# Performance work log

Hardware: AMD Instinct MI355X
Metric: run time of the kernel (lower is better)

Reference implementation:

```python
import jax, jax.numpy as jnp
import numpy as np

OUT_DIM = 130

def _gru_cell(x, h, wih, whh, bih, bhh):
    # torch.nn.GRUCell math
    gi = x @ wih.T + bih            # [N, 3H]
    gh = h @ whh.T + bhh            # [N, 3H]
    ir, iz, inn = jnp.split(gi, 3, axis=-1)
    hr, hz, hn = jnp.split(gh, 3, axis=-1)
    r = jax.nn.sigmoid(ir + hr)
    z = jax.nn.sigmoid(iz + hz)
    n = jnp.tanh(inn + r * hn)
    return (1.0 - z) * n + z * h


def setup_inputs() -> dict:
    key = jax.random.key(0)
    ks = jax.random.split(key, 16)
    E, B, C, H, D = 16, 128, 512, 1024, OUT_DIM
    S = 16  # length // 2
    T = E * S
    s = 0.02
    inp = {
        "c": jax.random.normal(ks[0], (E, B, C), jnp.float32),
        "target": jax.random.normal(ks[1], (B, T, D), jnp.float32),
        "length": 32,
        "batch_size": B,
        "fc_init_w": s * jax.random.normal(ks[2], (2 * H, C), jnp.float32),
        "fc_init_b": s * jax.random.normal(ks[3], (2 * H,), jnp.float32),
        "g1_wih": s * jax.random.normal(ks[4], (3 * H, C + D), jnp.float32),
        "g1_whh": s * jax.random.normal(ks[5], (3 * H, H), jnp.float32),
        "g1_bih": s * jax.random.normal(ks[6], (3 * H,), jnp.float32),
        "g1_bhh": s * jax.random.normal(ks[7], (3 * H,), jnp.float32),
        "g2_wih": s * jax.random.normal(ks[8], (3 * H, H), jnp.float32),
        "g2_whh": s * jax.random.normal(ks[9], (3 * H, H), jnp.float32),
        "g2_bih": s * jax.random.normal(ks[10], (3 * H,), jnp.float32),
        "g2_bhh": s * jax.random.normal(ks[11], (3 * H,), jnp.float32),
        "fco_w": s * jax.random.normal(ks[12], (D, H), jnp.float32),
        "fco_b": s * jax.random.normal(ks[13], (D,), jnp.float32),
    }
    return inp


def reference(c, target, length, batch_size, fc_init_w, fc_init_b,
              g1_wih, g1_whh, g1_bih, g1_bhh,
              g2_wih, g2_whh, g2_bih, g2_bhh, fco_w, fco_b):
    E, B, C = c.shape
    H = fc_init_w.shape[0] // 2
    D = fco_w.shape[0]
    S = length // 2
    T = E * S
    # h1/h2 init per conductor embed: tanh(fc_init(embed))
    t0 = jnp.tanh(c @ fc_init_w.T + fc_init_b)           # [E,B,2H]
    h1 = t0[..., :H].reshape(E * B, H)
    h2 = t0[..., H:].reshape(E * B, H)
    # teacher-forced previous: prev[t]=0 at t=0 else target[:,t-1]
    prev = jnp.concatenate([jnp.zeros((B, 1, D), target.dtype), target[:, :T - 1]], axis=1)  # [B,T,D]
    # global step t = e*S + s -> [S, E*B, D]
    prev = prev.transpose(1, 0, 2).reshape(E, S, B, D).transpose(1, 0, 2, 3).reshape(S, E * B, D)
    cflat = c.reshape(E * B, C)

    def step(carry, prev_t):
        h1, h2 = carry
        x = jnp.concatenate([cflat, prev_t], axis=-1)    # [E*B, C+D]
        h1 = _gru_cell(x, h1, g1_wih, g1_whh, g1_bih, g1_bhh)
        h2 = _gru_cell(h1, h2, g2_wih, g2_whh, g2_bih, g2_bhh)
        y = h2 @ fco_w.T + fco_b                         # [E*B, D]
        return (h1, h2), y

    _, ys = jax.lax.scan(step, (h1, h2), prev)           # [S, E*B, D]
    ys = ys.reshape(S, E, B, D).transpose(2, 1, 0, 3).reshape(B, T, D)
    return ys
```

## Files before the change

kernel.cpp:

```cpp
#include <hip/hip_runtime.h>

typedef unsigned short u16;
typedef __attribute__((ext_vector_type(8))) short frag8;
typedef __attribute__((ext_vector_type(4))) float f32x4;
typedef __attribute__((ext_vector_type(8))) unsigned short u16x8;

typedef __attribute__((address_space(1))) const void GV;
typedef __attribute__((address_space(3))) void LV;

__device__ __forceinline__ void gl16(const u16* g, u16* l) {
  __builtin_amdgcn_global_load_lds((GV*)g, (LV*)l, 16, 0, 0);
}

__device__ __forceinline__ float b2f(u16 u) {
  union { unsigned int i; float f; } v; v.i = ((unsigned int)u) << 16; return v.f;
}
__device__ __forceinline__ u16 f2b(float f) {
  union { float f; unsigned int i; } v; v.f = f;
  unsigned int x = v.i;
  x += 0x7fffu + ((x >> 16) & 1u);
  return (u16)(x >> 16);
}
__device__ __forceinline__ float ftanh(float x) {
  float e = __expf(2.f * x);
  return 1.f - 2.f / (e + 1.f);
}

__device__ __forceinline__ void xcd_remap(int axis, int& bx, int& by) {
  const int nx = gridDim.x, ny = gridDim.y;
  const int nwg = nx * ny;
  const int bid = blockIdx.x + nx * blockIdx.y;
  const int q = nwg >> 3, r = nwg & 7;
  const int xcd = bid & 7, i = bid >> 3;
  const int rem = (xcd < r ? xcd * (q + 1) : r * (q + 1) + (xcd - r) * q) + i;
  if (axis == 0) { bx = rem / ny; by = rem - bx * ny; }
  else           { by = rem / nx; bx = rem - by * nx; }
}

__global__ void cvt3(const float* __restrict__ s0, const float* __restrict__ s1,
                     const float* __restrict__ s2, u16* __restrict__ d0,
                     u16* __restrict__ d1, u16* __restrict__ d2) {
  int i = blockIdx.x * 256 + threadIdx.x;
  int which = i / 3145728;
  int j = i - which * 3145728;
  const float* s = (which == 0) ? s0 : (which == 1 ? s1 : s2);
  u16* d = (which == 0) ? d0 : (which == 1 ? d1 : d2);
  d[j] = f2b(s[j]);
}

__global__ void cvt2(const float* __restrict__ s0, const float* __restrict__ s1,
                     u16* __restrict__ d0, u16* __restrict__ d1) {
  int i = blockIdx.x * 256 + threadIdx.x;
  if (i < 1048576) d0[i] = f2b(s0[i]);
  else             d1[i - 1048576] = f2b(s1[i - 1048576]);
}

__global__ void prep_w1(const float* __restrict__ wih, u16* __restrict__ Wc, u16* __restrict__ Wd) {
  int i = blockIdx.x * 256 + threadIdx.x;
  const int NC = 3072 * 512;
  const int ND = 3072 * 192;
  if (i < NC) {
    int n = i >> 9, k = i & 511;
    Wc[i] = f2b(wih[n * 642 + k]);
  } else if (i < NC + ND) {
    int j = i - NC;
    int n = j / 192, k = j - n * 192;
    Wd[j] = (k < 130) ? f2b(wih[n * 642 + 512 + k]) : (u16)0;
  }
}

__global__ void prep_wby(const float* __restrict__ fcow, u16* __restrict__ wby) {
  int i = blockIdx.x * 256 + threadIdx.x;
  int n = i >> 10;
  wby[i] = (n < 130) ? f2b(fcow[i]) : (u16)0;
}

__global__ void prep_prev(const float* __restrict__ target, u16* __restrict__ P) {
  int i = blockIdx.x * 256 + threadIdx.x;
  int row = i / 24;
  int c8  = i - row * 24;
  int k0 = c8 * 8;
  int t = row >> 11, m2 = row & 2047;
  int e = m2 >> 7, b = m2 & 127;
  int tt = e * 16 + t;
  u16x8 r;
  if (tt > 0 && k0 + 8 <= 130) {
    const float* trow = target + (size_t)(b * 256 + tt - 1) * 130 + k0;
#pragma unroll
    for (int q = 0; q < 8; ++q) r[q] = f2b(trow[q]);
  } else if (tt > 0 && k0 < 130) {
    const float* trow = target + (size_t)(b * 256 + tt - 1) * 130;
#pragma unroll
    for (int q = 0; q < 8; ++q) { int k = k0 + q; r[q] = (k < 130) ? f2b(trow[k]) : (u16)0; }
  } else {
#pragma unroll
    for (int q = 0; q < 8; ++q) r[q] = (u16)0;
  }
  *(u16x8*)&P[(size_t)row * 192 + k0] = r;
}

__device__ __forceinline__ void kloop3(
    const u16* gA, const u16* gB, int nk,
    u16* AsBase, u16* BsBase, int wave,
    int rdA, int rdB, f32x4 (&acc)[2][4])
{
  u16* Adst = AsBase + wave * 512;
  u16* Bdst = BsBase + wave * 512;
  gl16(gA,      Adst);        gl16(gB,      Bdst);
  gl16(gA + 32, Adst + 4096); gl16(gB + 32, Bdst + 4096);
  const u16* pA = gA + 64;
  const u16* pB = gB + 64;
  int cbuf = 0, nbuf = 2;
  for (int ks = 0; ks < nk; ++ks) {
    if (ks < nk - 1) asm volatile("s_waitcnt vmcnt(2)" : : : "memory");
    else             asm volatile("s_waitcnt vmcnt(0)" : : : "memory");
    __builtin_amdgcn_s_barrier();
    __builtin_amdgcn_sched_barrier(0);
    if (ks + 2 < nk) {
      gl16(pA, Adst + nbuf * 4096);
      gl16(pB, Bdst + nbuf * 4096);
      pA += 32; pB += 32;
    }
    const u16* Ab = AsBase + cbuf * 4096;
    const u16* Bb = BsBase + cbuf * 4096;
    frag8 af[2], bfr[4];
#pragma unroll
    for (int i = 0; i < 2; ++i)
      af[i] = *(const frag8*)&Ab[rdA + i * 512];
#pragma unroll
    for (int j = 0; j < 4; ++j)
      bfr[j] = *(const frag8*)&Bb[rdB + j * 512];
#pragma unroll
    for (int i = 0; i < 2; ++i)
#pragma unroll
      for (int j = 0; j < 4; ++j)
        acc[i][j] = __builtin_amdgcn_mfma_f32_16x16x32_bf16(af[i], bfr[j], acc[i][j], 0, 0, 0);
    cbuf = (cbuf == 2) ? 0 : cbuf + 1;
    nbuf = (nbuf == 2) ? 0 : nbuf + 1;
  }
}

__global__ __launch_bounds__(512, 6) void gemm_bt(
    const u16* __restrict__ A, int lda,
    const u16* __restrict__ B0, const u16* __restrict__ B1, int ldb, int n_split,
    int N, int K, int mode, int tstep, int axis,
    const float* __restrict__ bias0, const float* __restrict__ bias1,
    u16* __restrict__ out0, u16* __restrict__ out1,
    const u16* __restrict__ addmat,
    float* __restrict__ fout0, float* __restrict__ fout1)
{
  __shared__ u16 As[3 * 4096];
  __shared__ u16 Bs[3 * 4096];

  int bx, by;
  xcd_remap(axis, bx, by);

  const int tid = threadIdx.x;
  const int wave = tid >> 6;
  const int lane = tid & 63;
  const int m0 = by * 128;
  const int n0 = bx * 128;
  const int wm = (wave & 3) * 32;
  const int wn = (wave >> 2) * 64;
  const int lr = lane & 15;
  const int lq = lane >> 4;
  const int sw = (lr >> 1) & 3;
  const int rdA = (wm + lr) * 32 + ((lq ^ sw) << 3);
  const int rdB = (wn + lr) * 32 + ((lq ^ sw) << 3);

  const u16* Bsel;
  int nb0;
  if (n0 < n_split) { Bsel = B0; nb0 = n0; }
  else              { Bsel = B1; nb0 = n0 - n_split; }

  f32x4 acc[2][4] = {};

  const int srow_g = wave * 16 + (lane >> 2);
  const int scol_g = (((lane & 3) ^ ((lane >> 3) & 3)) << 3);
  const u16* gA = &A[(size_t)(m0 + srow_g) * lda + scol_g];
  const u16* gB = &Bsel[(size_t)(nb0 + srow_g) * ldb + scol_g];

  kloop3(gA, gB, K >> 5, As, Bs, wave, rdA, rdB, acc);

#pragma unroll
  for (int i = 0; i < 2; ++i) {
#pragma unroll
    for (int r = 0; r < 4; ++r) {
      int m = m0 + wm + i * 16 + lq * 4 + r;
#pragma unroll
      for (int j = 0; j < 4; ++j) {
        int n = n0 + wn + j * 16 + lr;
        float v = acc[i][j][r];
        if (mode == 1) {
          float t = ftanh(v + bias0[n]);
          if (n < 1024) { fout0[(size_t)m * 1024 + n] = t;          out0[(size_t)m * 1024 + n] = f2b(t); }
          else          { fout1[(size_t)m * 1024 + (n - 1024)] = t; out1[(size_t)m * 1024 + (n - 1024)] = f2b(t); }
        } else if (mode == 2) {
          out0[(size_t)m * 3072 + n] = f2b(v + b2f(addmat[(size_t)(m & 2047) * 3072 + n]));
        } else if (mode == 3) {
          if (n < 3072) out0[(size_t)m * 3072 + n] = f2b(v + bias0[n]);
          else          out1[(size_t)m * 3072 + (n - 3072)] = f2b(v + bias1[n - 3072]);
        } else {
          if (n < 3072) {
            out0[(size_t)m * 3072 + n] = f2b(v + bias0[n]);
          } else if (n < 3202) {
            int d = n - 3072;
            int b = m & 127, e = m >> 7;
            fout0[(size_t)((b << 8) + (e << 4) + tstep) * 130 + d] = v + bias1[d];
          }
        }
      }
    }
  }
}

__global__ __launch_bounds__(512, 6) void gemm_init(
    const u16* __restrict__ cbf, const u16* __restrict__ h1b, const u16* __restrict__ h2b,
    const u16* __restrict__ Wc, const u16* __restrict__ W1h, const u16* __restrict__ W2h,
    const float* __restrict__ b1ih, const float* __restrict__ b1hh, const float* __restrict__ b2hh,
    u16* __restrict__ gic, u16* __restrict__ gh1, u16* __restrict__ gh2)
{
  __shared__ u16 As[3 * 4096];
  __shared__ u16 Bs[3 * 4096];

  int bx, by;
  xcd_remap(0, bx, by);

  const int tid = threadIdx.x;
  const int wave = tid >> 6;
  const int lane = tid & 63;
  const int m0 = by * 128;
  const int reg = bx / 24;
  const int nb0 = (bx - reg * 24) * 128;
  const int wm = (wave & 3) * 32;
  const int wn = (wave >> 2) * 64;
  const int lr = lane & 15;
  const int lq = lane >> 4;
  const int sw = (lr >> 1) & 3;
  const int rdA = (wm + lr) * 32 + ((lq ^ sw) << 3);
  const int rdB = (wn + lr) * 32 + ((lq ^ sw) << 3);

  const u16* A    = (reg == 0) ? cbf : (reg == 1) ? h1b : h2b;
  const u16* Bw   = (reg == 0) ? Wc  : (reg == 1) ? W1h : W2h;
  const float* bi = (reg == 0) ? b1ih : (reg == 1) ? b1hh : b2hh;
  u16* out        = (reg == 0) ? gic : (reg == 1) ? gh1 : gh2;
  const int ld    = (reg == 0) ? 512 : 1024;
  const int K     = (reg == 0) ? 512 : 1024;

  const int srow_g = wave * 16 + (lane >> 2);
  const int scol_g = (((lane & 3) ^ ((lane >> 3) & 3)) << 3);
  const u16* gA = &A[(size_t)(m0 + srow_g) * ld + scol_g];
  const u16* gB = &Bw[(size_t)(nb0 + srow_g) * ld + scol_g];

  f32x4 acc[2][4] = {};
  kloop3(gA, gB, K >> 5, As, Bs, wave, rdA, rdB, acc);

#pragma unroll
  for (int i = 0; i < 2; ++i) {
#pragma unroll
    for (int r = 0; r < 4; ++r) {
      int m = m0 + wm + i * 16 + lq * 4 + r;
#pragma unroll
      for (int j = 0; j < 4; ++j) {
        int n = nb0 + wn + j * 16 + lr;
        out[(size_t)m * 3072 + n] = f2b(acc[i][j][r] + bi[n]);
      }
    }
  }
}

__global__ __launch_bounds__(512, 6) void gemm_fused(
    const u16* __restrict__ A1, const u16* __restrict__ A2,
    const u16* __restrict__ W2i, const u16* __restrict__ W1h,
    const u16* __restrict__ W2h, const u16* __restrict__ WBy,
    const float* __restrict__ b_gi2, const float* __restrict__ b_gh1,
    const float* __restrict__ b_gh2, const float* __restrict__ b_y,
    u16* __restrict__ gi2, u16* __restrict__ gh1, u16* __restrict__ gh2,
    float* __restrict__ y, int tstep)
{
  __shared__ u16 As[3 * 4096];
  __shared__ u16 Bs[3 * 4096];

  int bx, by;
  xcd_remap(0, bx, by);

  const int tid = threadIdx.x;
  const int wave = tid >> 6;
  const int lane = tid & 63;
  const int m0 = by * 128;
  const int n0 = bx * 128;
  const int wm = (wave & 3) * 32;
  const int wn = (wave >> 2) * 64;
  const int lr = lane & 15;
  const int lq = lane >> 4;
  const int sw = (lr >> 1) & 3;
  const int rdA = (wm + lr) * 32 + ((lq ^ sw) << 3);
  const int rdB = (wn + lr) * 32 + ((lq ^ sw) << 3);

  const int reg = (n0 >= 9216) ? 3 : (n0 / 3072);
  const int nb0 = n0 - reg * 3072;
  const u16* A  = (reg < 2) ? A1 : A2;
  const u16* Bw = (reg == 0) ? W2i : (reg == 1) ? W1h : (reg == 2) ? W2h : WBy;
  const float* bias = (reg == 0) ? b_gi2 : (reg == 1) ? b_gh1 : (reg == 2) ? b_gh2 : b_y;

  const int srow_g = wave * 16 + (lane >> 2);
  const int scol_g = (((lane & 3) ^ ((lane >> 3) & 3)) << 3);
  const u16* gA = &A[(size_t)(m0 + srow_g) * 1024 + scol_g];
  const u16* gB = &Bw[(size_t)(nb0 + srow_g) * 1024 + scol_g];

  f32x4 acc[2][4] = {};
  kloop3(gA, gB, 32, As, Bs, wave, rdA, rdB, acc);

#pragma unroll
  for (int i = 0; i < 2; ++i) {
#pragma unroll
    for (int r = 0; r < 4; ++r) {
      int m = m0 + wm + i * 16 + lq * 4 + r;
#pragma unroll
      for (int j = 0; j < 4; ++j) {
        int nl = nb0 + wn + j * 16 + lr;
        float v = acc[i][j][r];
        if (reg == 0)      gi2[(size_t)m * 3072 + nl] = f2b(v + bias[nl]);
        else if (reg == 1) gh1[(size_t)m * 3072 + nl] = f2b(v + bias[nl]);
        else if (reg == 2) gh2[(size_t)m * 3072 + nl] = f2b(v + bias[nl]);
        else if (nl < 130) {
          int b = m & 127, e = m >> 7;
          y[(size_t)((b << 8) + (e << 4) + tstep) * 130 + nl] = v + bias[nl];
        }
      }
    }
  }
}

__global__ __launch_bounds__(256) void gru2(
    const u16* __restrict__ giA, const u16* __restrict__ ghA,
    float* __restrict__ hA, u16* __restrict__ hbA,
    const u16* __restrict__ giB, const u16* __restrict__ ghB,
    float* __restrict__ hB, u16* __restrict__ hbB,
    int doA, int doB)
{
  int blk = blockIdx.x;
  const u16 *gi, *gh; float* h32; u16* hb16;
  if (blk < 1024) { if (!doA) return; gi = giA; gh = ghA; h32 = hA; hb16 = hbA; }
  else { if (!doB) return; gi = giB; gh = ghB; h32 = hB; hb16 = hbB; blk -= 1024; }
  int idx = blk * 256 + threadIdx.x;
  int m = idx >> 7;
  int j0 = (idx & 127) << 3;
  const size_t gb = (size_t)m * 3072 + j0;
  const size_t hb = (size_t)m * 1024 + j0;
  u16x8 ir = *(const u16x8*)&gi[gb];
  u16x8 iz = *(const u16x8*)&gi[gb + 1024];
  u16x8 in_ = *(const u16x8*)&gi[gb + 2048];
  u16x8 hr = *(const u16x8*)&gh[gb];
  u16x8 hz = *(const u16x8*)&gh[gb + 1024];
  u16x8 hn = *(const u16x8*)&gh[gb + 2048];
  f32x4 h0 = *(const f32x4*)&h32[hb];
  f32x4 h1v = *(const f32x4*)&h32[hb + 4];
  f32x4 o0, o1;
  u16x8 ob;
#pragma unroll
  for (int q = 0; q < 8; ++q) {
    float r = 1.f / (1.f + __expf(-(b2f(ir[q]) + b2f(hr[q]))));
    float z = 1.f / (1.f + __expf(-(b2f(iz[q]) + b2f(hz[q]))));
    float nn = ftanh(b2f(in_[q]) + r * b2f(hn[q]));
    float hh = (q < 4) ? h0[q & 3] : h1v[q & 3];
    float res = (1.f - z) * nn + z * hh;
    if (q < 4) o0[q & 3] = res; else o1[q & 3] = res;
    ob[q] = f2b(res);
  }
  *(f32x4*)&h32[hb] = o0;
  *(f32x4*)&h32[hb + 4] = o1;
  *(u16x8*)&hb16[hb] = ob;
}

extern "C" void kernel_launch(void* const* d_in, const int* in_sizes, int n_in,
                              void* d_out, int out_size, void* d_ws, size_t ws_size,
                              hipStream_t stream)
{
  const float* c      = (const float*)d_in[0];
  const float* target = (const float*)d_in[1];
  const float* fiw    = (const float*)d_in[4];
  const float* fib    = (const float*)d_in[5];
  const float* g1wih  = (const float*)d_in[6];
  const float* g1whh  = (const float*)d_in[7];
  const float* g1bih  = (const float*)d_in[8];
  const float* g1bhh  = (const float*)d_in[9];
  const float* g2wih  = (const float*)d_in[10];
  const float* g2whh  = (const float*)d_in[11];
  const float* g2bih  = (const float*)d_in[12];
  const float* g2bhh  = (const float*)d_in[13];
  const float* fcow   = (const float*)d_in[14];
  const float* fcob   = (const float*)d_in[15];
  float* out = (float*)d_out;

  char* wsp = (char*)d_ws;
  size_t off = 0;
  auto takeb = [&](size_t bytes) {
    void* p = (void*)(wsp + off);
    off += bytes;
    off = (off + 255) & ~(size_t)255;
    return p;
  };
  float* h1f = (float*)takeb((size_t)2048 * 1024 * 4);
  float* h2f = (float*)takeb((size_t)2048 * 1024 * 4);
  u16* h1b   = (u16*)takeb((size_t)2048 * 1024 * 2);
  u16* h2b   = (u16*)takeb((size_t)2048 * 1024 * 2);
  u16* gic   = (u16*)takeb((size_t)2048 * 3072 * 2);
  u16* gib   = (u16*)takeb((size_t)2048 * 3072 * 2);
  u16* gh1   = (u16*)takeb((size_t)2048 * 3072 * 2);
  u16* gh2   = (u16*)takeb((size_t)2048 * 3072 * 2);
  u16* cbf   = (u16*)takeb((size_t)2048 * 512 * 2);
  u16* Wfi   = (u16*)takeb((size_t)2048 * 512 * 2);
  u16* Wc    = (u16*)takeb((size_t)3072 * 512 * 2);
  u16* Wd    = (u16*)takeb((size_t)3072 * 192 * 2);
  u16* W1h   = (u16*)takeb((size_t)3072 * 1024 * 2);
  u16* W2i   = (u16*)takeb((size_t)3072 * 1024 * 2);
  u16* W2h   = (u16*)takeb((size_t)3072 * 1024 * 2);
  u16* WBy   = (u16*)takeb((size_t)256 * 1024 * 2);
  u16* P     = (u16*)takeb((size_t)32768 * 192 * 2);
  const size_t GI1_BYTES = (size_t)16 * 2048 * 3072 * 2;
  u16* gi1 = nullptr;
  if (ws_size >= off + GI1_BYTES + 256) gi1 = (u16*)takeb(GI1_BYTES);
  (void)in_sizes; (void)n_in; (void)out_size;

  const int BIG = 1 << 30;

  cvt2<<<8192, 256, 0, stream>>>(c, fiw, cbf, Wfi);
  cvt3<<<36864, 256, 0, stream>>>(g1whh, g2wih, g2whh, W1h, W2i, W2h);
  prep_w1 <<<8448, 256, 0, stream>>>(g1wih, Wc, Wd);
  prep_wby<<<1024, 256, 0, stream>>>(fcow, WBy);
  prep_prev<<<3072, 256, 0, stream>>>(target, P);

  gemm_bt<<<dim3(16, 16), 512, 0, stream>>>(cbf, 512, Wfi, nullptr, 512, BIG,
                                            2048, 512, 1, 0, 0, fib, nullptr,
                                            h1b, h2b, nullptr, h1f, h2f);
  gemm_init<<<dim3(72, 16), 512, 0, stream>>>(cbf, h1b, h2b, Wc, W1h, W2h,
                                              g1bih, g1bhh, g2bhh, gic, gh1, gh2);

  if (gi1 != nullptr) {
    gemm_bt<<<dim3(24, 256), 512, 0, stream>>>(P, 192, Wd, nullptr, 192, BIG,
                                               3072, 192, 2, 0, 1, nullptr, nullptr,
                                               gi1, nullptr, gic, nullptr, nullptr);

    gru2<<<2048, 256, 0, stream>>>(gi1, gh1, h1f, h1b, nullptr, nullptr, nullptr, nullptr, 1, 0);
    gemm_bt<<<dim3(48, 16), 512, 0, stream>>>(h1b, 1024, W2i, W1h, 1024, 3072,
                                              6144, 1024, 3, 0, 0, g2bih, g1bhh,
                                              gib, gh1, nullptr, nullptr, nullptr);
    for (int t = 1; t < 16; ++t) {
      gru2<<<2048, 256, 0, stream>>>(gi1 + (size_t)t * 2048 * 3072, gh1, h1f, h1b,
                                     gib, gh2, h2f, h2b, 1, 1);
      gemm_fused<<<dim3(74, 16), 512, 0, stream>>>(h1b, h2b, W2i, W1h, W2h, WBy,
                                                   g2bih, g1bhh, g2bhh, fcob,
                                                   gib, gh1, gh2, out, t - 1);
    }
    gru2<<<2048, 256, 0, stream>>>(nullptr, nullptr, nullptr, nullptr,
                                   gib, gh2, h2f, h2b, 0, 1);
    gemm_bt<<<dim3(26, 16), 512, 0, stream>>>(h2b, 1024, W2h, WBy, 1024, 3072,
                                              3328, 1024, 4, 15, 0, g2bhh, fcob,
                                              gh2, nullptr, nullptr, out, nullptr);
  } else {
    for (int t = 0; t < 16; ++t) {
      gemm_bt<<<dim3(24, 16), 512, 0, stream>>>(P + (size_t)t * 2048 * 192, 192, Wd, nullptr, 192, BIG,
                                                3072, 192, 2, 0, 0, nullptr, nullptr,
                                                gib, nullptr, gic, nullptr, nullptr);
      gru2<<<2048, 256, 0, stream>>>(gib, gh1, h1f, h1b, nullptr, nullptr, nullptr, nullptr, 1, 0);
      gemm_bt<<<dim3(48, 16), 512, 0, stream>>>(h1b, 1024, W2i, W1h, 1024, 3072,
                                                6144, 1024, 3, 0, 0, g2bih, g1bhh,
                                                gib, gh1, nullptr, nullptr, nullptr);
      gru2<<<2048, 256, 0, stream>>>(gib, gh2, h2f, h2b, nullptr, nullptr, nullptr, nullptr, 1, 0);
      gemm_bt<<<dim3(26, 16), 512, 0, stream>>>(h2b, 1024, W2h, WBy, 1024, 3072,
                                                3328, 1024, 4, t, 0, g2bhh, fcob,
                                                gh2, nullptr, nullptr, out, nullptr);
    }
  }
}
```

Baseline: 1.892 ms.

## Fuse prep kernels and compute per-step input projection inside fused GEMM

```diff
diff --git a/kernel.cpp b/kernel.cpp
--- a/kernel.cpp
+++ b/kernel.cpp
@@ -37,66 +37,56 @@
   else           { by = rem / nx; bx = rem - by * nx; }
 }
 
-__global__ void cvt3(const float* __restrict__ s0, const float* __restrict__ s1,
-                     const float* __restrict__ s2, u16* __restrict__ d0,
-                     u16* __restrict__ d1, u16* __restrict__ d2) {
+__global__ void mega_prep(const float* __restrict__ c, const float* __restrict__ fiw,
+                          const float* __restrict__ g1whh, const float* __restrict__ g2wih,
+                          const float* __restrict__ g2whh, const float* __restrict__ g1wih,
+                          const float* __restrict__ fcow, const float* __restrict__ target,
+                          u16* __restrict__ cbf, u16* __restrict__ Wfi, u16* __restrict__ W1h,
+                          u16* __restrict__ W2i, u16* __restrict__ W2h, u16* __restrict__ Wc,
+                          u16* __restrict__ Wd, u16* __restrict__ WBy, u16* __restrict__ P)
+{
   int i = blockIdx.x * 256 + threadIdx.x;
-  int which = i / 3145728;
-  int j = i - which * 3145728;
-  const float* s = (which == 0) ? s0 : (which == 1 ? s1 : s2);
-  u16* d = (which == 0) ? d0 : (which == 1 ? d1 : d2);
-  d[j] = f2b(s[j]);
-}
-
-__global__ void cvt2(const float* __restrict__ s0, const float* __restrict__ s1,
-                     u16* __restrict__ d0, u16* __restrict__ d1) {
-  int i = blockIdx.x * 256 + threadIdx.x;
-  if (i < 1048576) d0[i] = f2b(s0[i]);
-  else             d1[i - 1048576] = f2b(s1[i - 1048576]);
-}
-
-__global__ void prep_w1(const float* __restrict__ wih, u16* __restrict__ Wc, u16* __restrict__ Wd) {
-  int i = blockIdx.x * 256 + threadIdx.x;
-  const int NC = 3072 * 512;
-  const int ND = 3072 * 192;
-  if (i < NC) {
-    int n = i >> 9, k = i & 511;
-    Wc[i] = f2b(wih[n * 642 + k]);
-  } else if (i < NC + ND) {
-    int j = i - NC;
-    int n = j / 192, k = j - n * 192;
-    Wd[j] = (k < 130) ? f2b(wih[n * 642 + 512 + k]) : (u16)0;
-  }
-}
-
-__global__ void prep_wby(const float* __restrict__ fcow, u16* __restrict__ wby) {
-  int i = blockIdx.x * 256 + threadIdx.x;
-  int n = i >> 10;
-  wby[i] = (n < 130) ? f2b(fcow[i]) : (u16)0;
-}
-
-__global__ void prep_prev(const float* __restrict__ target, u16* __restrict__ P) {
-  int i = blockIdx.x * 256 + threadIdx.x;
-  int row = i / 24;
-  int c8  = i - row * 24;
-  int k0 = c8 * 8;
-  int t = row >> 11, m2 = row & 2047;
-  int e = m2 >> 7, b = m2 & 127;
-  int tt = e * 16 + t;
-  u16x8 r;
-  if (tt > 0 && k0 + 8 <= 130) {
-    const float* trow = target + (size_t)(b * 256 + tt - 1) * 130 + k0;
-#pragma unroll
-    for (int q = 0; q < 8; ++q) r[q] = f2b(trow[q]);
-  } else if (tt > 0 && k0 < 130) {
-    const float* trow = target + (size_t)(b * 256 + tt - 1) * 130;
-#pragma unroll
-    for (int q = 0; q < 8; ++q) { int k = k0 + q; r[q] = (k < 130) ? f2b(trow[k]) : (u16)0; }
-  } else {
-#pragma unroll
-    for (int q = 0; q < 8; ++q) r[q] = (u16)0;
-  }
-  *(u16x8*)&P[(size_t)row * 192 + k0] = r;
+  if (i < 1048576) { cbf[i] = f2b(c[i]); return; }
+  i -= 1048576;
+  if (i < 1048576) { Wfi[i] = f2b(fiw[i]); return; }
+  i -= 1048576;
+  if (i < 3145728) { W1h[i] = f2b(g1whh[i]); return; }
+  i -= 3145728;
+  if (i < 3145728) { W2i[i] = f2b(g2wih[i]); return; }
+  i -= 3145728;
+  if (i < 3145728) { W2h[i] = f2b(g2whh[i]); return; }
+  i -= 3145728;
+  if (i < 1572864) { int n = i >> 9, k = i & 511; Wc[i] = f2b(g1wih[n * 642 + k]); return; }
+  i -= 1572864;
+  if (i < 589824) {
+    int n = i / 192, k = i - n * 192;
+    Wd[i] = (k < 130) ? f2b(g1wih[n * 642 + 512 + k]) : (u16)0;
+    return;
+  }
+  i -= 589824;
+  if (i < 262144) { int n = i >> 10; WBy[i] = (n < 130) ? f2b(fcow[i]) : (u16)0; return; }
+  i -= 262144;
+  {
+    int row = i / 24;
+    int k0 = (i - row * 24) * 8;
+    int t = row >> 11, m2 = row & 2047;
+    int e = m2 >> 7, b = m2 & 127;
+    int tt = e * 16 + t;
+    u16x8 r;
+    if (tt > 0 && k0 + 8 <= 130) {
+      const float* trow = target + (size_t)(b * 256 + tt - 1) * 130 + k0;
+#pragma unroll
+      for (int q = 0; q < 8; ++q) r[q] = f2b(trow[q]);
+    } else if (tt > 0 && k0 < 130) {
+      const float* trow = target + (size_t)(b * 256 + tt - 1) * 130;
+#pragma unroll
+      for (int q = 0; q < 8; ++q) { int k = k0 + q; r[q] = (k < 130) ? f2b(trow[k]) : (u16)0; }
+    } else {
+#pragma unroll
+      for (int q = 0; q < 8; ++q) r[q] = (u16)0;
+    }
+    *(u16x8*)&P[(size_t)row * 192 + k0] = r;
+  }
 }
 
 __device__ __forceinline__ void kloop3(
@@ -140,6 +130,20 @@
   }
 }
 
+struct GeomT { int wave, lane, wm, wn, lr, lq, rdA, rdB, srow, scol; };
+__device__ __forceinline__ GeomT geom(int tid) {
+  GeomT g;
+  g.wave = tid >> 6; g.lane = tid & 63;
+  g.wm = (g.wave & 3) * 32; g.wn = (g.wave >> 2) * 64;
+  g.lr = g.lane & 15; g.lq = g.lane >> 4;
+  int sw = (g.lr >> 1) & 3;
+  g.rdA = (g.wm + g.lr) * 32 + ((g.lq ^ sw) << 3);
+  g.rdB = (g.wn + g.lr) * 32 + ((g.lq ^ sw) << 3);
+  g.srow = g.wave * 16 + (g.lane >> 2);
+  g.scol = (((g.lane & 3) ^ ((g.lane >> 3) & 3)) << 3);
+  return g;
+}
+
 __global__ __launch_bounds__(512, 6) void gemm_bt(
     const u16* __restrict__ A, int lda,
     const u16* __restrict__ B0, const u16* __restrict__ B1, int ldb, int n_split,
@@ -151,51 +155,29 @@
 {
   __shared__ u16 As[3 * 4096];
   __shared__ u16 Bs[3 * 4096];
-
-  int bx, by;
-  xcd_remap(axis, bx, by);
-
-  const int tid = threadIdx.x;
-  const int wave = tid >> 6;
-  const int lane = tid & 63;
-  const int m0 = by * 128;
-  const int n0 = bx * 128;
-  const int wm = (wave & 3) * 32;
-  const int wn = (wave >> 2) * 64;
-  const int lr = lane & 15;
-  const int lq = lane >> 4;
-  const int sw = (lr >> 1) & 3;
-  const int rdA = (wm + lr) * 32 + ((lq ^ sw) << 3);
-  const int rdB = (wn + lr) * 32 + ((lq ^ sw) << 3);
-
-  const u16* Bsel;
-  int nb0;
+  int bx, by; xcd_remap(axis, bx, by);
+  GeomT g = geom(threadIdx.x);
+  const int m0 = by * 128, n0 = bx * 128;
+
+  const u16* Bsel; int nb0;
   if (n0 < n_split) { Bsel = B0; nb0 = n0; }
   else              { Bsel = B1; nb0 = n0 - n_split; }
 
   f32x4 acc[2][4] = {};
-
-  const int srow_g = wave * 16 + (lane >> 2);
-  const int scol_g = (((lane & 3) ^ ((lane >> 3) & 3)) << 3);
-  const u16* gA = &A[(size_t)(m0 + srow_g) * lda + scol_g];
-  const u16* gB = &Bsel[(size_t)(nb0 + srow_g) * ldb + scol_g];
-
-  kloop3(gA, gB, K >> 5, As, Bs, wave, rdA, rdB, acc);
+  const u16* gA = &A[(size_t)(m0 + g.srow) * lda + g.scol];
+  const u16* gB = &Bsel[(size_t)(nb0 + g.srow) * ldb + g.scol];
+  kloop3(gA, gB, K >> 5, As, Bs, g.wave, g.rdA, g.rdB, acc);
 
 #pragma unroll
   for (int i = 0; i < 2; ++i) {
 #pragma unroll
     for (int r = 0; r < 4; ++r) {
-      int m = m0 + wm + i * 16 + lq * 4 + r;
+      int m = m0 + g.wm + i * 16 + g.lq * 4 + r;
 #pragma unroll
       for (int j = 0; j < 4; ++j) {
-        int n = n0 + wn + j * 16 + lr;
+        int n = n0 + g.wn + j * 16 + g.lr;
         float v = acc[i][j][r];
-        if (mode == 1) {
-          float t = ftanh(v + bias0[n]);
-          if (n < 1024) { fout0[(size_t)m * 1024 + n] = t;          out0[(size_t)m * 1024 + n] = f2b(t); }
-          else          { fout1[(size_t)m * 1024 + (n - 1024)] = t; out1[(size_t)m * 1024 + (n - 1024)] = f2b(t); }
-        } else if (mode == 2) {
+        if (mode == 2) {
           out0[(size_t)m * 3072 + n] = f2b(v + b2f(addmat[(size_t)(m & 2047) * 3072 + n]));
         } else if (mode == 3) {
           if (n < 3072) out0[(size_t)m * 3072 + n] = f2b(v + bias0[n]);
@@ -214,118 +196,135 @@
   }
 }
 
-__global__ __launch_bounds__(512, 6) void gemm_init(
-    const u16* __restrict__ cbf, const u16* __restrict__ h1b, const u16* __restrict__ h2b,
-    const u16* __restrict__ Wc, const u16* __restrict__ W1h, const u16* __restrict__ W2h,
-    const float* __restrict__ b1ih, const float* __restrict__ b1hh, const float* __restrict__ b2hh,
-    u16* __restrict__ gic, u16* __restrict__ gh1, u16* __restrict__ gh2)
+__global__ __launch_bounds__(512, 6) void gemm_A(
+    const u16* __restrict__ cbf, const u16* __restrict__ Wfi, const u16* __restrict__ Wc,
+    const float* __restrict__ fib, const float* __restrict__ g1bih,
+    float* __restrict__ h1f, float* __restrict__ h2f,
+    u16* __restrict__ h1b, u16* __restrict__ h2b, u16* __restrict__ gic)
 {
   __shared__ u16 As[3 * 4096];
   __shared__ u16 Bs[3 * 4096];
-
-  int bx, by;
-  xcd_remap(0, bx, by);
-
-  const int tid = threadIdx.x;
-  const int wave = tid >> 6;
-  const int lane = tid & 63;
+  int bx, by; xcd_remap(0, bx, by);
+  GeomT g = geom(threadIdx.x);
   const int m0 = by * 128;
-  const int reg = bx / 24;
-  const int nb0 = (bx - reg * 24) * 128;
-  const int wm = (wave & 3) * 32;
-  const int wn = (wave >> 2) * 64;
-  const int lr = lane & 15;
-  const int lq = lane >> 4;
-  const int sw = (lr >> 1) & 3;
-  const int rdA = (wm + lr) * 32 + ((lq ^ sw) << 3);
-  const int rdB = (wn + lr) * 32 + ((lq ^ sw) << 3);
-
-  const u16* A    = (reg == 0) ? cbf : (reg == 1) ? h1b : h2b;
-  const u16* Bw   = (reg == 0) ? Wc  : (reg == 1) ? W1h : W2h;
-  const float* bi = (reg == 0) ? b1ih : (reg == 1) ? b1hh : b2hh;
-  u16* out        = (reg == 0) ? gic : (reg == 1) ? gh1 : gh2;
-  const int ld    = (reg == 0) ? 512 : 1024;
-  const int K     = (reg == 0) ? 512 : 1024;
-
-  const int srow_g = wave * 16 + (lane >> 2);
-  const int scol_g = (((lane & 3) ^ ((lane >> 3) & 3)) << 3);
-  const u16* gA = &A[(size_t)(m0 + srow_g) * ld + scol_g];
-  const u16* gB = &Bw[(size_t)(nb0 + srow_g) * ld + scol_g];
+  const int isInit = (bx < 16);
+  const int nb0 = isInit ? bx * 128 : (bx - 16) * 128;
+  const u16* Bw = isInit ? Wfi : Wc;
 
   f32x4 acc[2][4] = {};
-  kloop3(gA, gB, K >> 5, As, Bs, wave, rdA, rdB, acc);
+  const u16* gA = &cbf[(size_t)(m0 + g.srow) * 512 + g.scol];
+  const u16* gB = &Bw[(size_t)(nb0 + g.srow) * 512 + g.scol];
+  kloop3(gA, gB, 16, As, Bs, g.wave, g.rdA, g.rdB, acc);
 
 #pragma unroll
   for (int i = 0; i < 2; ++i) {
 #pragma unroll
     for (int r = 0; r < 4; ++r) {
-      int m = m0 + wm + i * 16 + lq * 4 + r;
+      int m = m0 + g.wm + i * 16 + g.lq * 4 + r;
 #pragma unroll
       for (int j = 0; j < 4; ++j) {
-        int n = nb0 + wn + j * 16 + lr;
-        out[(size_t)m * 3072 + n] = f2b(acc[i][j][r] + bi[n]);
+        int n = nb0 + g.wn + j * 16 + g.lr;
+        float v = acc[i][j][r];
+        if (isInit) {
+          float t = ftanh(v + fib[n]);
+          if (n < 1024) { h1f[(size_t)m * 1024 + n] = t;          h1b[(size_t)m * 1024 + n] = f2b(t); }
+          else          { h2f[(size_t)m * 1024 + (n - 1024)] = t; h2b[(size_t)m * 1024 + (n - 1024)] = f2b(t); }
+        } else {
+          gic[(size_t)m * 3072 + n] = f2b(v + g1bih[n]);
+        }
       }
     }
   }
 }
 
+__global__ __launch_bounds__(512, 6) void gemm_B(
+    const u16* __restrict__ h1b, const u16* __restrict__ h2b, const u16* __restrict__ P,
+    const u16* __restrict__ W1h, const u16* __restrict__ W2h, const u16* __restrict__ Wd,
+    const float* __restrict__ b1hh, const float* __restrict__ b2hh,
+    const u16* __restrict__ gic,
+    u16* __restrict__ gh1, u16* __restrict__ gh2, u16* __restrict__ gi1w)
+{
+  __shared__ u16 As[3 * 4096];
+  __shared__ u16 Bs[3 * 4096];
+  int bx, by; xcd_remap(0, bx, by);
+  GeomT g = geom(threadIdx.x);
+  const int m0 = by * 128;
+  int reg, nb0;
+  const u16 *A, *Bw; int ld, K;
+  if (bx < 24)      { reg = 0; nb0 = bx * 128;        A = h1b; Bw = W1h; ld = 1024; K = 1024; }
+  else if (bx < 48) { reg = 1; nb0 = (bx - 24) * 128; A = h2b; Bw = W2h; ld = 1024; K = 1024; }
+  else              { reg = 2; nb0 = (bx - 48) * 128; A = P;   Bw = Wd;  ld = 192;  K = 192;  }
+
+  f32x4 acc[2][4] = {};
+  const u16* gA = &A[(size_t)(m0 + g.srow) * ld + g.scol];
+  const u16* gB = &Bw[(size_t)(nb0 + g.srow) * ld + g.scol];
+  kloop3(gA, gB, K >> 5, As, Bs, g.wave, g.rdA, g.rdB, acc);
+
+#pragma unroll
+  for (int i = 0; i < 2; ++i) {
+#pragma unroll
+    for (int r = 0; r < 4; ++r) {
+      int m = m0 + g.wm + i * 16 + g.lq * 4 + r;
+#pragma unroll
+      for (int j = 0; j < 4; ++j) {
+        int n = nb0 + g.wn + j * 16 + g.lr;
+        float v = acc[i][j][r];
+        if (reg == 0)      gh1[(size_t)m * 3072 + n] = f2b(v + b1hh[n]);
+        else if (reg == 1) gh2[(size_t)m * 3072 + n] = f2b(v + b2hh[n]);
+        else               gi1w[(size_t)m * 3072 + n] = f2b(v + b2f(gic[(size_t)m * 3072 + n]));
+      }
+    }
+  }
+}
+
 __global__ __launch_bounds__(512, 6) void gemm_fused(
-    const u16* __restrict__ A1, const u16* __restrict__ A2,
-    const u16* __restrict__ W2i, const u16* __restrict__ W1h,
-    const u16* __restrict__ W2h, const u16* __restrict__ WBy,
+    const u16* __restrict__ h1b, const u16* __restrict__ h2b, const u16* __restrict__ Pt,
+    const u16* __restrict__ W2i, const u16* __restrict__ W1h, const u16* __restrict__ W2h,
+    const u16* __restrict__ WBy, const u16* __restrict__ Wd,
     const float* __restrict__ b_gi2, const float* __restrict__ b_gh1,
     const float* __restrict__ b_gh2, const float* __restrict__ b_y,
+    const u16* __restrict__ gic,
     u16* __restrict__ gi2, u16* __restrict__ gh1, u16* __restrict__ gh2,
-    float* __restrict__ y, int tstep)
+    float* __restrict__ y, u16* __restrict__ gi1w,
+    int c0, int c1, int c2, int c3, int tstep)
 {
   __shared__ u16 As[3 * 4096];
   __shared__ u16 Bs[3 * 4096];
-
-  int bx, by;
-  xcd_remap(0, bx, by);
-
-  const int tid = threadIdx.x;
-  const int wave = tid >> 6;
-  const int lane = tid & 63;
+  int bx, by; xcd_remap(0, bx, by);
+  GeomT g = geom(threadIdx.x);
   const int m0 = by * 128;
-  const int n0 = bx * 128;
-  const int wm = (wave & 3) * 32;
-  const int wn = (wave >> 2) * 64;
-  const int lr = lane & 15;
-  const int lq = lane >> 4;
-  const int sw = (lr >> 1) & 3;
-  const int rdA = (wm + lr) * 32 + ((lq ^ sw) << 3);
-  const int rdB = (wn + lr) * 32 + ((lq ^ sw) << 3);
-
-  const int reg = (n0 >= 9216) ? 3 : (n0 / 3072);
-  const int nb0 = n0 - reg * 3072;
-  const u16* A  = (reg < 2) ? A1 : A2;
-  const u16* Bw = (reg == 0) ? W2i : (reg == 1) ? W1h : (reg == 2) ? W2h : WBy;
-  const float* bias = (reg == 0) ? b_gi2 : (reg == 1) ? b_gh1 : (reg == 2) ? b_gh2 : b_y;
-
-  const int srow_g = wave * 16 + (lane >> 2);
-  const int scol_g = (((lane & 3) ^ ((lane >> 3) & 3)) << 3);
-  const u16* gA = &A[(size_t)(m0 + srow_g) * 1024 + scol_g];
-  const u16* gB = &Bw[(size_t)(nb0 + srow_g) * 1024 + scol_g];
+  int reg, nb0;
+  const u16 *A, *Bw; int ld, K;
+  if (bx < c0)      { reg = 0; nb0 = bx * 128;        A = h1b; Bw = W2i; ld = 1024; K = 1024; }
+  else if (bx < c1) { reg = 1; nb0 = (bx - c0) * 128; A = h1b; Bw = W1h; ld = 1024; K = 1024; }
+  else if (bx < c2) { reg = 2; nb0 = (bx - c1) * 128; A = h2b; Bw = W2h; ld = 1024; K = 1024; }
+  else if (bx < c3) { reg = 3; nb0 = (bx - c2) * 128; A = h2b; Bw = WBy; ld = 1024; K = 1024; }
+  else              { reg = 4; nb0 = (bx - c3) * 128; A = Pt;  Bw = Wd;  ld = 192;  K = 192;  }
 
   f32x4 acc[2][4] = {};
-  kloop3(gA, gB, 32, As, Bs, wave, rdA, rdB, acc);
+  const u16* gA = &A[(size_t)(m0 + g.srow) * ld + g.scol];
+  const u16* gB = &Bw[(size_t)(nb0 + g.srow) * ld + g.scol];
+  kloop3(gA, gB, K >> 5, As, Bs, g.wave, g.rdA, g.rdB, acc);
 
 #pragma unroll
   for (int i = 0; i < 2; ++i) {
 #pragma unroll
     for (int r = 0; r < 4; ++r) {
-      int m = m0 + wm + i * 16 + lq * 4 + r;
+      int m = m0 + g.wm + i * 16 + g.lq * 4 + r;
 #pragma unroll
       for (int j = 0; j < 4; ++j) {
-        int nl = nb0 + wn + j * 16 + lr;
+        int nl = nb0 + g.wn + j * 16 + g.lr;
         float v = acc[i][j][r];
-        if (reg == 0)      gi2[(size_t)m * 3072 + nl] = f2b(v + bias[nl]);
-        else if (reg == 1) gh1[(size_t)m * 3072 + nl] = f2b(v + bias[nl]);
-        else if (reg == 2) gh2[(size_t)m * 3072 + nl] = f2b(v + bias[nl]);
-        else if (nl < 130) {
-          int b = m & 127, e = m >> 7;
-          y[(size_t)((b << 8) + (e << 4) + tstep) * 130 + nl] = v + bias[nl];
+        if (reg == 0)      gi2[(size_t)m * 3072 + nl] = f2b(v + b_gi2[nl]);
+        else if (reg == 1) gh1[(size_t)m * 3072 + nl] = f2b(v + b_gh1[nl]);
+        else if (reg == 2) gh2[(size_t)m * 3072 + nl] = f2b(v + b_gh2[nl]);
+        else if (reg == 3) {
+          if (nl < 130) {
+            int b = m & 127, e = m >> 7;
+            y[(size_t)((b << 8) + (e << 4) + tstep) * 130 + nl] = v + b_y[nl];
+          }
+        } else {
+          gi1w[(size_t)m * 3072 + nl] = f2b(v + b2f(gic[(size_t)m * 3072 + nl]));
         }
       }
     }
@@ -418,47 +417,50 @@
   u16* W2h   = (u16*)takeb((size_t)3072 * 1024 * 2);
   u16* WBy   = (u16*)takeb((size_t)256 * 1024 * 2);
   u16* P     = (u16*)takeb((size_t)32768 * 192 * 2);
-  const size_t GI1_BYTES = (size_t)16 * 2048 * 3072 * 2;
-  u16* gi1 = nullptr;
-  if (ws_size >= off + GI1_BYTES + 256) gi1 = (u16*)takeb(GI1_BYTES);
+  u16* g1A = nullptr;
+  if (ws_size >= off + (size_t)2048 * 3072 * 2 + 256) g1A = (u16*)takeb((size_t)2048 * 3072 * 2);
   (void)in_sizes; (void)n_in; (void)out_size;
 
   const int BIG = 1 << 30;
 
-  cvt2<<<8192, 256, 0, stream>>>(c, fiw, cbf, Wfi);
-  cvt3<<<36864, 256, 0, stream>>>(g1whh, g2wih, g2whh, W1h, W2i, W2h);
-  prep_w1 <<<8448, 256, 0, stream>>>(g1wih, Wc, Wd);
-  prep_wby<<<1024, 256, 0, stream>>>(fcow, WBy);
-  prep_prev<<<3072, 256, 0, stream>>>(target, P);
-
-  gemm_bt<<<dim3(16, 16), 512, 0, stream>>>(cbf, 512, Wfi, nullptr, 512, BIG,
-                                            2048, 512, 1, 0, 0, fib, nullptr,
-                                            h1b, h2b, nullptr, h1f, h2f);
-  gemm_init<<<dim3(72, 16), 512, 0, stream>>>(cbf, h1b, h2b, Wc, W1h, W2h,
-                                              g1bih, g1bhh, g2bhh, gic, gh1, gh2);
-
-  if (gi1 != nullptr) {
-    gemm_bt<<<dim3(24, 256), 512, 0, stream>>>(P, 192, Wd, nullptr, 192, BIG,
-                                               3072, 192, 2, 0, 1, nullptr, nullptr,
-                                               gi1, nullptr, gic, nullptr, nullptr);
-
-    gru2<<<2048, 256, 0, stream>>>(gi1, gh1, h1f, h1b, nullptr, nullptr, nullptr, nullptr, 1, 0);
-    gemm_bt<<<dim3(48, 16), 512, 0, stream>>>(h1b, 1024, W2i, W1h, 1024, 3072,
-                                              6144, 1024, 3, 0, 0, g2bih, g1bhh,
-                                              gib, gh1, nullptr, nullptr, nullptr);
-    for (int t = 1; t < 16; ++t) {
-      gru2<<<2048, 256, 0, stream>>>(gi1 + (size_t)t * 2048 * 3072, gh1, h1f, h1b,
-                                     gib, gh2, h2f, h2b, 1, 1);
-      gemm_fused<<<dim3(74, 16), 512, 0, stream>>>(h1b, h2b, W2i, W1h, W2h, WBy,
-                                                   g2bih, g1bhh, g2bhh, fcob,
-                                                   gib, gh1, gh2, out, t - 1);
-    }
+  mega_prep<<<57600, 256, 0, stream>>>(c, fiw, g1whh, g2wih, g2whh, g1wih, fcow, target,
+                                       cbf, Wfi, W1h, W2i, W2h, Wc, Wd, WBy, P);
+  gemm_A<<<dim3(40, 16), 512, 0, stream>>>(cbf, Wfi, Wc, fib, g1bih,
+                                           h1f, h2f, h1b, h2b, gic);
+
+  if (g1A != nullptr) {
+    gemm_B<<<dim3(72, 16), 512, 0, stream>>>(h1b, h2b, P, W1h, W2h, Wd,
+                                             g1bhh, g2bhh, gic, gh1, gh2, g1A);
+    gru2<<<2048, 256, 0, stream>>>(g1A, gh1, h1f, h1b, nullptr, nullptr, nullptr, nullptr, 1, 0);
+    gemm_fused<<<dim3(72, 16), 512, 0, stream>>>(h1b, h2b, P + (size_t)1 * 2048 * 192,
+                                                 W2i, W1h, W2h, WBy, Wd,
+                                                 g2bih, g1bhh, g2bhh, fcob, gic,
+                                                 gib, gh1, gh2, out, g1A,
+                                                 24, 48, 48, 48, 0);
+    for (int t = 1; t <= 14; ++t) {
+      gru2<<<2048, 256, 0, stream>>>(g1A, gh1, h1f, h1b, gib, gh2, h2f, h2b, 1, 1);
+      gemm_fused<<<dim3(98, 16), 512, 0, stream>>>(h1b, h2b, P + (size_t)(t + 1) * 2048 * 192,
+                                                   W2i, W1h, W2h, WBy, Wd,
+                                                   g2bih, g1bhh, g2bhh, fcob, gic,
+                                                   gib, gh1, gh2, out, g1A,
+                                                   24, 48, 72, 74, t - 1);
+    }
+    gru2<<<2048, 256, 0, stream>>>(g1A, gh1, h1f, h1b, gib, gh2, h2f, h2b, 1, 1);
+    gemm_fused<<<dim3(50, 16), 512, 0, stream>>>(h1b, h2b, P,
+                                                 W2i, W1h, W2h, WBy, Wd,
+                                                 g2bih, g1bhh, g2bhh, fcob, gic,
+                                                 gib, gh1, gh2, out, g1A,
+                                                 24, 24, 48, 50, 14);
     gru2<<<2048, 256, 0, stream>>>(nullptr, nullptr, nullptr, nullptr,
                                    gib, gh2, h2f, h2b, 0, 1);
-    gemm_bt<<<dim3(26, 16), 512, 0, stream>>>(h2b, 1024, W2h, WBy, 1024, 3072,
-                                              3328, 1024, 4, 15, 0, g2bhh, fcob,
-                                              gh2, nullptr, nullptr, out, nullptr);
+    gemm_fused<<<dim3(2, 16), 512, 0, stream>>>(h1b, h2b, P,
+                                                W2i, W1h, W2h, WBy, Wd,
+                                                g2bih, g1bhh, g2bhh, fcob, gic,
+                                                gib, gh1, gh2, out, g1A,
+                                                0, 0, 0, 2, 15);
   } else {
+    gemm_B<<<dim3(48, 16), 512, 0, stream>>>(h1b, h2b, P, W1h, W2h, Wd,
+                                             g1bhh, g2bhh, gic, gh1, gh2, nullptr);
     for (int t = 0; t < 16; ++t) {
       gemm_bt<<<dim3(24, 16), 512, 0, stream>>>(P + (size_t)t * 2048 * 192, 192, Wd, nullptr, 192, BIG,
                                                 3072, 192, 2, 0, 0, nullptr, nullptr,
```

Measured after the change: 1.803 ms. 4.7% less time.
